# Kernel optimization log

Hardware: AMD Instinct MI355X
Metric: run time of the kernel (lower is better)

The kernel has to match this reference:

```python
import jax, jax.numpy as jnp
import numpy as np

B, T, D_MODEL, D_HIDDEN, MAX_SEQLEN = 4, 2048, 1024, 256, 2048


def setup_inputs() -> dict:
    key = jax.random.key(0)
    ks = jax.random.split(key, 8)
    s_in = 1.0 / np.sqrt(D_MODEL)
    s_out = 1.0 / np.sqrt(D_HIDDEN)
    # xavier_uniform bound for W_bias (fan_in = fan_out = MAX_SEQLEN)
    xb = np.sqrt(6.0 / (MAX_SEQLEN + MAX_SEQLEN))
    return {
        "q": jax.random.normal(ks[0], (B, T, D_MODEL), jnp.float32),
        "k": jax.random.normal(ks[1], (B, T, D_MODEL), jnp.float32),
        "v": jax.random.normal(ks[2], (B, T, D_MODEL), jnp.float32),
        "Wq": jax.random.normal(ks[3], (D_MODEL, D_HIDDEN), jnp.float32) * s_in,
        "Wk": jax.random.normal(ks[4], (D_MODEL, D_HIDDEN), jnp.float32) * s_in,
        "Wv": jax.random.normal(ks[5], (D_MODEL, D_HIDDEN), jnp.float32) * s_in,
        "Wo": jax.random.normal(ks[6], (D_HIDDEN, D_MODEL), jnp.float32) * s_out,
        "W_bias": jax.random.uniform(ks[7], (MAX_SEQLEN, MAX_SEQLEN), jnp.float32, -xb, xb),
    }


def reference(q, k, v, Wq, Wk, Wv, Wo, W_bias):
    Ti, Tj = q.shape[1], k.shape[1]
    Q = q @ Wq                      # [B,Ti,dh]
    K = k @ Wk                      # [B,Tj,dh]
    V = v @ Wv                      # [B,Tj,dh]
    pos_bias = W_bias[:Ti, :Tj][None]               # [1,Ti,Tj]
    # NOTE: source subtracts max over dim 0 (batch). For pos_bias that dim is 1,
    # so exp_pos_bias == exp(0) == ones -- reproduced faithfully here.
    max_key = jnp.max(K, axis=0, keepdims=True)      # [1,Tj,dh]
    max_pos_bias = jnp.max(pos_bias, axis=0, keepdims=True)
    exp_key = jnp.exp(K - max_key)                   # [B,Tj,dh]
    exp_pos_bias = jnp.exp(pos_bias - max_pos_bias)  # [1,Ti,Tj]
    num = jnp.einsum('ij,bjd->bid', exp_pos_bias[0], exp_key * V)  # [B,Ti,dh]
    den = jnp.einsum('ij,bjd->bid', exp_pos_bias[0], exp_key)      # [B,Ti,dh]
    Yt = jax.nn.sigmoid(Q) * num / den
    return Yt @ Wo                  # [B,Ti,d_model]
```

## Files before the change

kernel.cpp:

```cpp
#include <hip/hip_runtime.h>
#include <hip/hip_bf16.h>
#include <math.h>

#define B_   4
#define T_   2048
#define DM   1024
#define DH   256
#define M_   (B_*T_)

typedef __bf16 bf16;
typedef __attribute__((ext_vector_type(8))) __bf16 bf16x8;
typedef __attribute__((ext_vector_type(4))) float  f32x4;

__device__ inline float sigmoidf_(float x) { return 1.0f / (1.0f + __expf(-x)); }

__device__ inline int swz8(int r, int c) { return (((c >> 3) ^ (r & 7)) << 3); }

__global__ void transpose_cvt_all(const float* __restrict__ Wq, const float* __restrict__ Wk,
                                  const float* __restrict__ Wv, const float* __restrict__ Wo,
                                  bf16* __restrict__ Wq_t, bf16* __restrict__ Wk_t,
                                  bf16* __restrict__ Wv_t, bf16* __restrict__ Wo_t)
{
    const int bid = blockIdx.x;
    __shared__ float tile[32][33];
    const int w = bid >> 8, t = bid & 255;
    const float* in; bf16* out; int R, C, sh;
    if      (w == 0) { in = Wq; out = Wq_t; R = DM; C = DH; sh = 3; }
    else if (w == 1) { in = Wk; out = Wk_t; R = DM; C = DH; sh = 3; }
    else if (w == 2) { in = Wv; out = Wv_t; R = DM; C = DH; sh = 3; }
    else             { in = Wo; out = Wo_t; R = DH; C = DM; sh = 5; }
    const int r0 = (t >> sh) * 32, c0 = (t & ((1 << sh) - 1)) * 32;
    const int tx = threadIdx.x & 31, ty = threadIdx.x >> 5;
    #pragma unroll
    for (int i = ty; i < 32; i += 8)
        tile[i][tx] = in[(long)(r0 + i) * C + c0 + tx];
    __syncthreads();
    #pragma unroll
    for (int i = ty; i < 32; i += 8)
        out[(long)(c0 + i) * R + r0 + tx] = (bf16)tile[tx][i];
}

#define GEMM_PHASE(APTR, WT, ACC) {                                           \
    const float* aBase = &(APTR)[arowg * DM + ac8];                           \
    const bf16*  bBase = &(WT)[(long)(n0 + br) * DM + bc16];                  \
    f32x4 pa0[2], pa1[2]; bf16x8 pb0[2], pb1[2];                              \
    _Pragma("unroll")                                                         \
    for (int p = 0; p < 2; ++p) {                                             \
        const float* ap = aBase + p * 64;                                     \
        pa0[p] = *(const f32x4*)ap; pa1[p] = *(const f32x4*)(ap + 4);         \
        const bf16* bp = bBase + p * 64;                                      \
        pb0[p] = *(const bf16x8*)bp; pb1[p] = *(const bf16x8*)(bp + 8);       \
    }                                                                         \
    {   bf16x8 o;                                                             \
        _Pragma("unroll")                                                     \
        for (int e = 0; e < 4; ++e) { o[e] = (bf16)pa0[0][e]; o[4+e] = (bf16)pa1[0][e]; } \
        *(bf16x8*)&As[0][ar][swz8(ar, ac8)]      = o;                         \
        *(bf16x8*)&Bs[0][br][swz8(br, bc16)]     = pb0[0];                    \
        *(bf16x8*)&Bs[0][br][swz8(br, bc16 + 8)] = pb1[0];                    \
    }                                                                         \
    __syncthreads();                                                          \
    _Pragma("unroll")                                                         \
    for (int s = 0; s < 16; ++s) {                                            \
        const int cs = s & 1, ns = cs ^ 1;                                    \
        if (s + 2 < 16) {                                                     \
            const float* ap = aBase + (s + 2) * 64;                           \
            pa0[cs] = *(const f32x4*)ap; pa1[cs] = *(const f32x4*)(ap + 4);   \
            const bf16* bp = bBase + (s + 2) * 64;                            \
            pb0[cs] = *(const bf16x8*)bp; pb1[cs] = *(const bf16x8*)(bp + 8); \
        }                                                                     \
        if (s + 1 < 16) {                                                     \
            bf16x8 o;                                                         \
            _Pragma("unroll")                                                 \
            for (int e = 0; e < 4; ++e) { o[e] = (bf16)pa0[ns][e]; o[4+e] = (bf16)pa1[ns][e]; } \
            *(bf16x8*)&As[ns][ar][swz8(ar, ac8)]      = o;                    \
            *(bf16x8*)&Bs[ns][br][swz8(br, bc16)]     = pb0[ns];              \
            *(bf16x8*)&Bs[ns][br][swz8(br, bc16 + 8)] = pb1[ns];              \
        }                                                                     \
        _Pragma("unroll")                                                     \
        for (int kk = 0; kk < 64; kk += 32) {                                 \
            const int ra = wr * 32 + l16, rb = wc * 32 + l16;                 \
            bf16x8 a0 = *(const bf16x8*)&As[cs][ra     ][swz8(ra,      kk + q4 * 8)]; \
            bf16x8 a1 = *(const bf16x8*)&As[cs][ra + 16][swz8(ra + 16, kk + q4 * 8)]; \
            bf16x8 b0 = *(const bf16x8*)&Bs[cs][rb     ][swz8(rb,      kk + q4 * 8)]; \
            bf16x8 b1 = *(const bf16x8*)&Bs[cs][rb + 16][swz8(rb + 16, kk + q4 * 8)]; \
            ACC[0][0] = __builtin_amdgcn_mfma_f32_16x16x32_bf16(a0, b0, ACC[0][0], 0, 0, 0); \
            ACC[0][1] = __builtin_amdgcn_mfma_f32_16x16x32_bf16(a0, b1, ACC[0][1], 0, 0, 0); \
            ACC[1][0] = __builtin_amdgcn_mfma_f32_16x16x32_bf16(a1, b0, ACC[1][0], 0, 0, 0); \
            ACC[1][1] = __builtin_amdgcn_mfma_f32_16x16x32_bf16(a1, b1, ACC[1][1], 0, 0, 0); \
        }                                                                     \
        __syncthreads();                                                      \
    } }

__global__ __launch_bounds__(512, 6)
void proj_fused(const float* __restrict__ qin, const float* __restrict__ kin,
                const float* __restrict__ vin,
                const bf16* __restrict__ Wq_t, const bf16* __restrict__ Wk_t,
                const bf16* __restrict__ Wv_t,
                bf16* __restrict__ Yb, float* __restrict__ part_num,
                float* __restrict__ part_den)
{
    __shared__ __align__(16) char smem[49152];
    auto As = reinterpret_cast<bf16 (*)[64][64]>(smem);
    auto Bs = reinterpret_cast<bf16 (*)[128][64]>(smem + 16384);

    const int z   = blockIdx.z;
    const int bid = blockIdx.x;
    const int tile = (bid & 7) * 32 + (bid >> 3);
    const int n0 = (tile & 1) * 128;

    const int tid = threadIdx.x, lane = tid & 63, wave = tid >> 6;
    const int wr = wave >> 2, wc = wave & 3;
    const int q4 = lane >> 4, l16 = lane & 15;
    const int ar = tid >> 3, ac8 = (tid & 7) * 8;
    const int br = tid >> 2, bc16 = (tid & 3) * 16;

    const int m0 = (tile >> 1) * 64;
    const int jt = tile >> 1;
    const long arowg = (z == 0) ? (long)(m0 + ar)
                                : (long)(ar >> 4) * T_ + jt * 16 + (ar & 15);

    f32x4 accA[2][2] = {};
    f32x4 accV[2][2] = {};

    if (z == 0) {
        GEMM_PHASE(qin, Wq_t, accA)
        #pragma unroll
        for (int i = 0; i < 2; ++i)
            #pragma unroll
            for (int j = 0; j < 2; ++j)
                #pragma unroll
                for (int r = 0; r < 4; ++r) {
                    int gm = m0 + wr * 32 + i * 16 + q4 * 4 + r;
                    int gn = n0 + wc * 32 + j * 16 + l16;
                    Yb[(long)gm * DH + gn] = (bf16)sigmoidf_(accA[i][j][r]);
                }
    } else {
        GEMM_PHASE(kin, Wk_t, accA)
        GEMM_PHASE(vin, Wv_t, accV)
        auto KL = reinterpret_cast<bf16 (*)[128]>(smem);
        auto VL = reinterpret_cast<bf16 (*)[128]>(smem + 16384);
        float* red_n = (float*)(smem + 32768);
        float* red_d = (float*)(smem + 40960);
        #pragma unroll
        for (int i = 0; i < 2; ++i)
            #pragma unroll
            for (int j = 0; j < 2; ++j)
                #pragma unroll
                for (int r = 0; r < 4; ++r) {
                    const int row = wr * 32 + i * 16 + q4 * 4 + r;
                    const int col = wc * 32 + j * 16 + l16;
                    KL[row][col] = (bf16)accA[i][j][r];
                    VL[row][col] = (bf16)accV[i][j][r];
                }
        __syncthreads();
        const int d = tid & 127, grp = tid >> 7;
        float sn0 = 0.f, sn1 = 0.f, sn2 = 0.f, sn3 = 0.f;
        float sd0 = 0.f, sd1 = 0.f, sd2 = 0.f, sd3 = 0.f;
        #pragma unroll
        for (int jj4 = 0; jj4 < 4; ++jj4) {
            const int jjj = grp * 4 + jj4;
            float k0 = (float)KL[jjj][d],      k1 = (float)KL[16 + jjj][d];
            float k2 = (float)KL[32 + jjj][d], k3 = (float)KL[48 + jjj][d];
            float mx = fmaxf(fmaxf(k0, k1), fmaxf(k2, k3));
            float e0 = __expf(k0 - mx), e1 = __expf(k1 - mx);
            float e2 = __expf(k2 - mx), e3 = __expf(k3 - mx);
            sn0 += e0 * (float)VL[jjj][d];      sd0 += e0;
            sn1 += e1 * (float)VL[16 + jjj][d]; sd1 += e1;
            sn2 += e2 * (float)VL[32 + jjj][d]; sd2 += e2;
            sn3 += e3 * (float)VL[48 + jjj][d]; sd3 += e3;
        }
        red_n[(grp * 4 + 0) * 128 + d] = sn0; red_d[(grp * 4 + 0) * 128 + d] = sd0;
        red_n[(grp * 4 + 1) * 128 + d] = sn1; red_d[(grp * 4 + 1) * 128 + d] = sd1;
        red_n[(grp * 4 + 2) * 128 + d] = sn2; red_d[(grp * 4 + 2) * 128 + d] = sd2;
        red_n[(grp * 4 + 3) * 128 + d] = sn3; red_d[(grp * 4 + 3) * 128 + d] = sd3;
        __syncthreads();
        {
            const int b = tid >> 7, dd = tid & 127;
            float num = red_n[(b) * 128 + dd]      + red_n[(4 + b) * 128 + dd]
                      + red_n[(8 + b) * 128 + dd]  + red_n[(12 + b) * 128 + dd];
            float den = red_d[(b) * 128 + dd]      + red_d[(4 + b) * 128 + dd]
                      + red_d[(8 + b) * 128 + dd]  + red_d[(12 + b) * 128 + dd];
            const int idx = ((jt * 4 + b) << 8) + n0 + dd;
            part_num[idx] = num;
            part_den[idx] = den;
        }
    }
}

__global__ void merge_kv(const float* __restrict__ pn, const float* __restrict__ pd,
                         float* __restrict__ rv)
{
    const int t = blockIdx.x * 256 + threadIdx.x;
    const int b = t >> 8, d = t & 255;
    float num = 0.f, den = 0.f;
    for (int jt = 0; jt < 128; ++jt) {
        num += pn[((jt * 4 + b) << 8) + d];
        den += pd[((jt * 4 + b) << 8) + d];
    }
    rv[t] = num / den;
}

__global__ __launch_bounds__(512, 6)
void gemm_out(const bf16* __restrict__ Yb, const bf16* __restrict__ Wo_t,
              const float* __restrict__ rv, float* __restrict__ out)
{
    __shared__ __align__(16) bf16 As[2][64][64];
    __shared__ __align__(16) bf16 Bs[2][128][64];
    __shared__ float rv_s[DH];

    const int bid  = blockIdx.x;
    const int tile = (bid & 7) * 128 + (bid >> 3);
    const int m0 = (tile >> 3) * 64;
    const int n0 = (tile & 7) * 128;
    const int b  = m0 >> 11;

    const int tid = threadIdx.x, lane = tid & 63, wave = tid >> 6;
    const int wr = wave >> 2, wc = wave & 3;
    const int q4 = lane >> 4, l16 = lane & 15;

    if (tid < DH) rv_s[tid] = rv[b * DH + tid];

    f32x4 acc[2][2] = {};
    const int ar = tid >> 3, ac8 = (tid & 7) * 8;
    const int br = tid >> 2, bc16 = (tid & 3) * 16;

    const bf16* aBase = &Yb[(long)(m0 + ar) * DH + ac8];
    const bf16* bBase = &Wo_t[(long)(n0 + br) * DH + bc16];

    bf16x8 pq[2], pb0[2], pb1[2];
    #pragma unroll
    for (int p = 0; p < 2; ++p) {
        pq[p]  = *(const bf16x8*)(aBase + p * 64);
        const bf16* wp = bBase + p * 64;
        pb0[p] = *(const bf16x8*)wp; pb1[p] = *(const bf16x8*)(wp + 8);
    }
    __syncthreads();
    {
        bf16x8 o;
        #pragma unroll
        for (int e = 0; e < 8; ++e)
            o[e] = (bf16)((float)pq[0][e] * rv_s[ac8 + e]);
        *(bf16x8*)&As[0][ar][swz8(ar, ac8)]      = o;
        *(bf16x8*)&Bs[0][br][swz8(br, bc16)]     = pb0[0];
        *(bf16x8*)&Bs[0][br][swz8(br, bc16 + 8)] = pb1[0];
    }
    __syncthreads();

    #pragma unroll
    for (int s = 0; s < 4; ++s) {
        const int cs = s & 1, ns = cs ^ 1;
        if (s + 2 < 4) {
            pq[cs]  = *(const bf16x8*)(aBase + (s + 2) * 64);
            const bf16* wp = bBase + (s + 2) * 64;
            pb0[cs] = *(const bf16x8*)wp; pb1[cs] = *(const bf16x8*)(wp + 8);
        }
        if (s + 1 < 4) {
            bf16x8 o;
            #pragma unroll
            for (int e = 0; e < 8; ++e)
                o[e] = (bf16)((float)pq[ns][e] * rv_s[(s + 1) * 64 + ac8 + e]);
            *(bf16x8*)&As[ns][ar][swz8(ar, ac8)]      = o;
            *(bf16x8*)&Bs[ns][br][swz8(br, bc16)]     = pb0[ns];
            *(bf16x8*)&Bs[ns][br][swz8(br, bc16 + 8)] = pb1[ns];
        }
        #pragma unroll
        for (int kk = 0; kk < 64; kk += 32) {
            const int ra = wr * 32 + l16, rb = wc * 32 + l16;
            bf16x8 a0 = *(const bf16x8*)&As[cs][ra     ][swz8(ra,      kk + q4 * 8)];
            bf16x8 a1 = *(const bf16x8*)&As[cs][ra + 16][swz8(ra + 16, kk + q4 * 8)];
            bf16x8 b0 = *(const bf16x8*)&Bs[cs][rb     ][swz8(rb,      kk + q4 * 8)];
            bf16x8 b1 = *(const bf16x8*)&Bs[cs][rb + 16][swz8(rb + 16, kk + q4 * 8)];
            acc[0][0] = __builtin_amdgcn_mfma_f32_16x16x32_bf16(a0, b0, acc[0][0], 0, 0, 0);
            acc[0][1] = __builtin_amdgcn_mfma_f32_16x16x32_bf16(a0, b1, acc[0][1], 0, 0, 0);
            acc[1][0] = __builtin_amdgcn_mfma_f32_16x16x32_bf16(a1, b0, acc[1][0], 0, 0, 0);
            acc[1][1] = __builtin_amdgcn_mfma_f32_16x16x32_bf16(a1, b1, acc[1][1], 0, 0, 0);
        }
        __syncthreads();
    }
    #pragma unroll
    for (int i = 0; i < 2; ++i)
        #pragma unroll
        for (int j = 0; j < 2; ++j)
            #pragma unroll
            for (int r = 0; r < 4; ++r) {
                int gm = m0 + wr * 32 + i * 16 + q4 * 4 + r;
                int gn = n0 + wc * 32 + j * 16 + l16;
                out[(long)gm * DM + gn] = acc[i][j][r];
            }
}

extern "C" void kernel_launch(void* const* d_in, const int* in_sizes, int n_in,
                              void* d_out, int out_size, void* d_ws, size_t ws_size,
                              hipStream_t stream)
{
    const float* q  = (const float*)d_in[0];
    const float* k  = (const float*)d_in[1];
    const float* v  = (const float*)d_in[2];
    const float* Wq = (const float*)d_in[3];
    const float* Wk = (const float*)d_in[4];
    const float* Wv = (const float*)d_in[5];
    const float* Wo = (const float*)d_in[6];
    float* out = (float*)d_out;

    char* ws = (char*)d_ws;
    bf16* Yb       = (bf16*)ws;  ws += (size_t)M_ * DH * sizeof(bf16);
    bf16* Wq_t     = (bf16*)ws;  ws += (size_t)DM * DH * sizeof(bf16);
    bf16* Wk_t     = (bf16*)ws;  ws += (size_t)DM * DH * sizeof(bf16);
    bf16* Wv_t     = (bf16*)ws;  ws += (size_t)DM * DH * sizeof(bf16);
    bf16* Wo_t     = (bf16*)ws;  ws += (size_t)DM * DH * sizeof(bf16);
    float* rv      = (float*)ws; ws += (size_t)B_ * DH * sizeof(float);
    float* part_n  = (float*)ws; ws += (size_t)128 * 4 * 256 * sizeof(float);
    float* part_d  = (float*)ws; ws += (size_t)128 * 4 * 256 * sizeof(float);

    transpose_cvt_all<<<1024, 256, 0, stream>>>(Wq, Wk, Wv, Wo,
                                                Wq_t, Wk_t, Wv_t, Wo_t);

    proj_fused<<<dim3(256, 1, 2), 512, 0, stream>>>(q, k, v, Wq_t, Wk_t, Wv_t,
                                                    Yb, part_n, part_d);
    merge_kv<<<4, 256, 0, stream>>>(part_n, part_d, rv);
    gemm_out<<<1024, 512, 0, stream>>>(Yb, Wo_t, rv, out);
}
```

Measured before the change: 195.9 us.

## Shrink GEMM N-tile to 64 to double block count and occupancy

Both the projection kernel and the output GEMM move from 64x128 tiles to 64x64 tiles, so the grids double (512x2 and 2048 blocks) and each wave issues 2 MFMAs per k-step instead of 4. Shared memory per block falls to 32KB and launch bounds rise to 8 blocks per CU, aiming for more parallelism and latency hiding on a chip with many CUs. The K/V reduction epilogue is reworked for the 64-column tile, and the z index that selects the Q path versus the K/V path is swapped. The cost is that the fp32 A-operand inputs (q, k, v) are reloaded and re-converted twice as often, and arithmetic intensity per block is lower.

```diff
diff --git a/kernel.cpp b/kernel.cpp
--- a/kernel.cpp
+++ b/kernel.cpp
@@ -40,23 +40,21 @@
         out[(long)(c0 + i) * R + r0 + tx] = (bf16)tile[tx][i];
 }
 
-#define GEMM_PHASE(APTR, WT, ACC) {                                           \
+#define GEMM_PHASE64(APTR, WT, ACC) {                                         \
     const float* aBase = &(APTR)[arowg * DM + ac8];                           \
-    const bf16*  bBase = &(WT)[(long)(n0 + br) * DM + bc16];                  \
-    f32x4 pa0[2], pa1[2]; bf16x8 pb0[2], pb1[2];                              \
+    const bf16*  bBase = &(WT)[(long)(n0 + ar) * DM + ac8];                   \
+    f32x4 pa0[2], pa1[2]; bf16x8 pb[2];                                       \
     _Pragma("unroll")                                                         \
     for (int p = 0; p < 2; ++p) {                                             \
         const float* ap = aBase + p * 64;                                     \
         pa0[p] = *(const f32x4*)ap; pa1[p] = *(const f32x4*)(ap + 4);         \
-        const bf16* bp = bBase + p * 64;                                      \
-        pb0[p] = *(const bf16x8*)bp; pb1[p] = *(const bf16x8*)(bp + 8);       \
+        pb[p]  = *(const bf16x8*)(bBase + p * 64);                            \
     }                                                                         \
     {   bf16x8 o;                                                             \
         _Pragma("unroll")                                                     \
         for (int e = 0; e < 4; ++e) { o[e] = (bf16)pa0[0][e]; o[4+e] = (bf16)pa1[0][e]; } \
-        *(bf16x8*)&As[0][ar][swz8(ar, ac8)]      = o;                         \
-        *(bf16x8*)&Bs[0][br][swz8(br, bc16)]     = pb0[0];                    \
-        *(bf16x8*)&Bs[0][br][swz8(br, bc16 + 8)] = pb1[0];                    \
+        *(bf16x8*)&As[0][ar][swz8(ar, ac8)] = o;                              \
+        *(bf16x8*)&Bs[0][ar][swz8(ar, ac8)] = pb[0];                          \
     }                                                                         \
     __syncthreads();                                                          \
     _Pragma("unroll")                                                         \
@@ -65,33 +63,28 @@
         if (s + 2 < 16) {                                                     \
             const float* ap = aBase + (s + 2) * 64;                           \
             pa0[cs] = *(const f32x4*)ap; pa1[cs] = *(const f32x4*)(ap + 4);   \
-            const bf16* bp = bBase + (s + 2) * 64;                            \
-            pb0[cs] = *(const bf16x8*)bp; pb1[cs] = *(const bf16x8*)(bp + 8); \
+            pb[cs]  = *(const bf16x8*)(bBase + (s + 2) * 64);                 \
         }                                                                     \
         if (s + 1 < 16) {                                                     \
             bf16x8 o;                                                         \
             _Pragma("unroll")                                                 \
             for (int e = 0; e < 4; ++e) { o[e] = (bf16)pa0[ns][e]; o[4+e] = (bf16)pa1[ns][e]; } \
-            *(bf16x8*)&As[ns][ar][swz8(ar, ac8)]      = o;                    \
-            *(bf16x8*)&Bs[ns][br][swz8(br, bc16)]     = pb0[ns];              \
-            *(bf16x8*)&Bs[ns][br][swz8(br, bc16 + 8)] = pb1[ns];              \
+            *(bf16x8*)&As[ns][ar][swz8(ar, ac8)] = o;                         \
+            *(bf16x8*)&Bs[ns][ar][swz8(ar, ac8)] = pb[ns];                    \
         }                                                                     \
         _Pragma("unroll")                                                     \
         for (int kk = 0; kk < 64; kk += 32) {                                 \
-            const int ra = wr * 32 + l16, rb = wc * 32 + l16;                 \
+            const int ra = wr * 32 + l16, rb = wc * 16 + l16;                 \
             bf16x8 a0 = *(const bf16x8*)&As[cs][ra     ][swz8(ra,      kk + q4 * 8)]; \
             bf16x8 a1 = *(const bf16x8*)&As[cs][ra + 16][swz8(ra + 16, kk + q4 * 8)]; \
             bf16x8 b0 = *(const bf16x8*)&Bs[cs][rb     ][swz8(rb,      kk + q4 * 8)]; \
-            bf16x8 b1 = *(const bf16x8*)&Bs[cs][rb + 16][swz8(rb + 16, kk + q4 * 8)]; \
-            ACC[0][0] = __builtin_amdgcn_mfma_f32_16x16x32_bf16(a0, b0, ACC[0][0], 0, 0, 0); \
-            ACC[0][1] = __builtin_amdgcn_mfma_f32_16x16x32_bf16(a0, b1, ACC[0][1], 0, 0, 0); \
-            ACC[1][0] = __builtin_amdgcn_mfma_f32_16x16x32_bf16(a1, b0, ACC[1][0], 0, 0, 0); \
-            ACC[1][1] = __builtin_amdgcn_mfma_f32_16x16x32_bf16(a1, b1, ACC[1][1], 0, 0, 0); \
+            ACC[0] = __builtin_amdgcn_mfma_f32_16x16x32_bf16(a0, b0, ACC[0], 0, 0, 0); \
+            ACC[1] = __builtin_amdgcn_mfma_f32_16x16x32_bf16(a1, b0, ACC[1], 0, 0, 0); \
         }                                                                     \
         __syncthreads();                                                      \
     } }
 
-__global__ __launch_bounds__(512, 6)
+__global__ __launch_bounds__(512, 8)
 void proj_fused(const float* __restrict__ qin, const float* __restrict__ kin,
                 const float* __restrict__ vin,
                 const bf16* __restrict__ Wq_t, const bf16* __restrict__ Wk_t,
@@ -99,87 +92,84 @@
                 bf16* __restrict__ Yb, float* __restrict__ part_num,
                 float* __restrict__ part_den)
 {
-    __shared__ __align__(16) char smem[49152];
+    __shared__ __align__(16) char smem[32768];
     auto As = reinterpret_cast<bf16 (*)[64][64]>(smem);
-    auto Bs = reinterpret_cast<bf16 (*)[128][64]>(smem + 16384);
+    auto Bs = reinterpret_cast<bf16 (*)[64][64]>(smem + 16384);
 
     const int z   = blockIdx.z;
     const int bid = blockIdx.x;
-    const int tile = (bid & 7) * 32 + (bid >> 3);
-    const int n0 = (tile & 1) * 128;
+    const int tile = (bid & 7) * 64 + (bid >> 3);
+    const int n0 = (tile & 3) * 64;
 
     const int tid = threadIdx.x, lane = tid & 63, wave = tid >> 6;
     const int wr = wave >> 2, wc = wave & 3;
     const int q4 = lane >> 4, l16 = lane & 15;
     const int ar = tid >> 3, ac8 = (tid & 7) * 8;
-    const int br = tid >> 2, bc16 = (tid & 3) * 16;
-
-    const int m0 = (tile >> 1) * 64;
-    const int jt = tile >> 1;
-    const long arowg = (z == 0) ? (long)(m0 + ar)
+
+    const int m0 = (tile >> 2) * 64;
+    const int jt = tile >> 2;
+    const long arowg = (z == 1) ? (long)(m0 + ar)
                                 : (long)(ar >> 4) * T_ + jt * 16 + (ar & 15);
 
-    f32x4 accA[2][2] = {};
-    f32x4 accV[2][2] = {};
-
-    if (z == 0) {
-        GEMM_PHASE(qin, Wq_t, accA)
+    f32x4 accA[2] = {};
+    f32x4 accV[2] = {};
+
+    if (z == 1) {
+        GEMM_PHASE64(qin, Wq_t, accA)
         #pragma unroll
         for (int i = 0; i < 2; ++i)
             #pragma unroll
-            for (int j = 0; j < 2; ++j)
-                #pragma unroll
-                for (int r = 0; r < 4; ++r) {
-                    int gm = m0 + wr * 32 + i * 16 + q4 * 4 + r;
-                    int gn = n0 + wc * 32 + j * 16 + l16;
-                    Yb[(long)gm * DH + gn] = (bf16)sigmoidf_(accA[i][j][r]);
-                }
+            for (int r = 0; r < 4; ++r) {
+                int gm = m0 + wr * 32 + i * 16 + q4 * 4 + r;
+                int gn = n0 + wc * 16 + l16;
+                Yb[(long)gm * DH + gn] = (bf16)sigmoidf_(accA[i][r]);
+            }
     } else {
-        GEMM_PHASE(kin, Wk_t, accA)
-        GEMM_PHASE(vin, Wv_t, accV)
-        auto KL = reinterpret_cast<bf16 (*)[128]>(smem);
-        auto VL = reinterpret_cast<bf16 (*)[128]>(smem + 16384);
-        float* red_n = (float*)(smem + 32768);
-        float* red_d = (float*)(smem + 40960);
+        GEMM_PHASE64(kin, Wk_t, accA)
+        GEMM_PHASE64(vin, Wv_t, accV)
+        auto KL = reinterpret_cast<bf16 (*)[64]>(smem);
+        auto VL = reinterpret_cast<bf16 (*)[64]>(smem + 8192);
+        float* red_n = (float*)(smem + 16384);
+        float* red_d = (float*)(smem + 24576);
         #pragma unroll
         for (int i = 0; i < 2; ++i)
             #pragma unroll
-            for (int j = 0; j < 2; ++j)
-                #pragma unroll
-                for (int r = 0; r < 4; ++r) {
-                    const int row = wr * 32 + i * 16 + q4 * 4 + r;
-                    const int col = wc * 32 + j * 16 + l16;
-                    KL[row][col] = (bf16)accA[i][j][r];
-                    VL[row][col] = (bf16)accV[i][j][r];
-                }
+            for (int r = 0; r < 4; ++r) {
+                const int row = wr * 32 + i * 16 + q4 * 4 + r;
+                const int col = wc * 16 + l16;
+                KL[row][col] = (bf16)accA[i][r];
+                VL[row][col] = (bf16)accV[i][r];
+            }
         __syncthreads();
-        const int d = tid & 127, grp = tid >> 7;
-        float sn0 = 0.f, sn1 = 0.f, sn2 = 0.f, sn3 = 0.f;
-        float sd0 = 0.f, sd1 = 0.f, sd2 = 0.f, sd3 = 0.f;
-        #pragma unroll
-        for (int jj4 = 0; jj4 < 4; ++jj4) {
-            const int jjj = grp * 4 + jj4;
-            float k0 = (float)KL[jjj][d],      k1 = (float)KL[16 + jjj][d];
-            float k2 = (float)KL[32 + jjj][d], k3 = (float)KL[48 + jjj][d];
+        const int d = tid & 63, grp = tid >> 6;
+        float sn[B_] = {}, sd[B_] = {};
+        #pragma unroll
+        for (int jj2 = 0; jj2 < 2; ++jj2) {
+            const int jj = grp * 2 + jj2;
+            float k0 = (float)KL[jj][d],      k1 = (float)KL[16 + jj][d];
+            float k2 = (float)KL[32 + jj][d], k3 = (float)KL[48 + jj][d];
             float mx = fmaxf(fmaxf(k0, k1), fmaxf(k2, k3));
             float e0 = __expf(k0 - mx), e1 = __expf(k1 - mx);
             float e2 = __expf(k2 - mx), e3 = __expf(k3 - mx);
-            sn0 += e0 * (float)VL[jjj][d];      sd0 += e0;
-            sn1 += e1 * (float)VL[16 + jjj][d]; sd1 += e1;
-            sn2 += e2 * (float)VL[32 + jjj][d]; sd2 += e2;
-            sn3 += e3 * (float)VL[48 + jjj][d]; sd3 += e3;
-        }
-        red_n[(grp * 4 + 0) * 128 + d] = sn0; red_d[(grp * 4 + 0) * 128 + d] = sd0;
-        red_n[(grp * 4 + 1) * 128 + d] = sn1; red_d[(grp * 4 + 1) * 128 + d] = sd1;
-        red_n[(grp * 4 + 2) * 128 + d] = sn2; red_d[(grp * 4 + 2) * 128 + d] = sd2;
-        red_n[(grp * 4 + 3) * 128 + d] = sn3; red_d[(grp * 4 + 3) * 128 + d] = sd3;
+            sn[0] += e0 * (float)VL[jj][d];      sd[0] += e0;
+            sn[1] += e1 * (float)VL[16 + jj][d]; sd[1] += e1;
+            sn[2] += e2 * (float)VL[32 + jj][d]; sd[2] += e2;
+            sn[3] += e3 * (float)VL[48 + jj][d]; sd[3] += e3;
+        }
+        #pragma unroll
+        for (int b = 0; b < B_; ++b) {
+            red_n[(b * 8 + grp) * 64 + d] = sn[b];
+            red_d[(b * 8 + grp) * 64 + d] = sd[b];
+        }
         __syncthreads();
-        {
-            const int b = tid >> 7, dd = tid & 127;
-            float num = red_n[(b) * 128 + dd]      + red_n[(4 + b) * 128 + dd]
-                      + red_n[(8 + b) * 128 + dd]  + red_n[(12 + b) * 128 + dd];
-            float den = red_d[(b) * 128 + dd]      + red_d[(4 + b) * 128 + dd]
-                      + red_d[(8 + b) * 128 + dd]  + red_d[(12 + b) * 128 + dd];
+        if (tid < 256) {
+            const int b = tid >> 6, dd = tid & 63;
+            float num = 0.f, den = 0.f;
+            #pragma unroll
+            for (int g = 0; g < 8; ++g) {
+                num += red_n[(b * 8 + g) * 64 + dd];
+                den += red_d[(b * 8 + g) * 64 + dd];
+            }
             const int idx = ((jt * 4 + b) << 8) + n0 + dd;
             part_num[idx] = num;
             part_den[idx] = den;
@@ -200,39 +190,38 @@
     rv[t] = num / den;
 }
 
-__global__ __launch_bounds__(512, 6)
+__global__ __launch_bounds__(512, 8)
 void gemm_out(const bf16* __restrict__ Yb, const bf16* __restrict__ Wo_t,
               const float* __restrict__ rv, float* __restrict__ out)
 {
-    __shared__ __align__(16) bf16 As[2][64][64];
-    __shared__ __align__(16) bf16 Bs[2][128][64];
+    __shared__ __align__(16) char smem[32768];
+    auto As = reinterpret_cast<bf16 (*)[64][64]>(smem);
+    auto Bs = reinterpret_cast<bf16 (*)[64][64]>(smem + 16384);
     __shared__ float rv_s[DH];
 
     const int bid  = blockIdx.x;
-    const int tile = (bid & 7) * 128 + (bid >> 3);
-    const int m0 = (tile >> 3) * 64;
-    const int n0 = (tile & 7) * 128;
+    const int tile = (bid & 7) * 256 + (bid >> 3);
+    const int m0 = (tile >> 4) * 64;
+    const int n0 = (tile & 15) * 64;
     const int b  = m0 >> 11;
 
     const int tid = threadIdx.x, lane = tid & 63, wave = tid >> 6;
     const int wr = wave >> 2, wc = wave & 3;
     const int q4 = lane >> 4, l16 = lane & 15;
+    const int ar = tid >> 3, ac8 = (tid & 7) * 8;
 
     if (tid < DH) rv_s[tid] = rv[b * DH + tid];
 
-    f32x4 acc[2][2] = {};
-    const int ar = tid >> 3, ac8 = (tid & 7) * 8;
-    const int br = tid >> 2, bc16 = (tid & 3) * 16;
+    f32x4 acc[2] = {};
 
     const bf16* aBase = &Yb[(long)(m0 + ar) * DH + ac8];
-    const bf16* bBase = &Wo_t[(long)(n0 + br) * DH + bc16];
-
-    bf16x8 pq[2], pb0[2], pb1[2];
+    const bf16* bBase = &Wo_t[(long)(n0 + ar) * DH + ac8];
+
+    bf16x8 pq[2], pb[2];
     #pragma unroll
     for (int p = 0; p < 2; ++p) {
-        pq[p]  = *(const bf16x8*)(aBase + p * 64);
-        const bf16* wp = bBase + p * 64;
-        pb0[p] = *(const bf16x8*)wp; pb1[p] = *(const bf16x8*)(wp + 8);
+        pq[p] = *(const bf16x8*)(aBase + p * 64);
+        pb[p] = *(const bf16x8*)(bBase + p * 64);
     }
     __syncthreads();
     {
@@ -240,9 +229,8 @@
         #pragma unroll
         for (int e = 0; e < 8; ++e)
             o[e] = (bf16)((float)pq[0][e] * rv_s[ac8 + e]);
-        *(bf16x8*)&As[0][ar][swz8(ar, ac8)]      = o;
-        *(bf16x8*)&Bs[0][br][swz8(br, bc16)]     = pb0[0];
-        *(bf16x8*)&Bs[0][br][swz8(br, bc16 + 8)] = pb1[0];
+        *(bf16x8*)&As[0][ar][swz8(ar, ac8)] = o;
+        *(bf16x8*)&Bs[0][ar][swz8(ar, ac8)] = pb[0];
     }
     __syncthreads();
 
@@ -250,43 +238,36 @@
     for (int s = 0; s < 4; ++s) {
         const int cs = s & 1, ns = cs ^ 1;
         if (s + 2 < 4) {
-            pq[cs]  = *(const bf16x8*)(aBase + (s + 2) * 64);
-            const bf16* wp = bBase + (s + 2) * 64;
-            pb0[cs] = *(const bf16x8*)wp; pb1[cs] = *(const bf16x8*)(wp + 8);
+            pq[cs] = *(const bf16x8*)(aBase + (s + 2) * 64);
+            pb[cs] = *(const bf16x8*)(bBase + (s + 2) * 64);
         }
         if (s + 1 < 4) {
             bf16x8 o;
             #pragma unroll
             for (int e = 0; e < 8; ++e)
                 o[e] = (bf16)((float)pq[ns][e] * rv_s[(s + 1) * 64 + ac8 + e]);
-            *(bf16x8*)&As[ns][ar][swz8(ar, ac8)]      = o;
-            *(bf16x8*)&Bs[ns][br][swz8(br, bc16)]     = pb0[ns];
-            *(bf16x8*)&Bs[ns][br][swz8(br, bc16 + 8)] = pb1[ns];
+            *(bf16x8*)&As[ns][ar][swz8(ar, ac8)] = o;
+            *(bf16x8*)&Bs[ns][ar][swz8(ar, ac8)] = pb[ns];
         }
         #pragma unroll
         for (int kk = 0; kk < 64; kk += 32) {
-            const int ra = wr * 32 + l16, rb = wc * 32 + l16;
+            const int ra = wr * 32 + l16, rb = wc * 16 + l16;
             bf16x8 a0 = *(const bf16x8*)&As[cs][ra     ][swz8(ra,      kk + q4 * 8)];
             bf16x8 a1 = *(const bf16x8*)&As[cs][ra + 16][swz8(ra + 16, kk + q4 * 8)];
             bf16x8 b0 = *(const bf16x8*)&Bs[cs][rb     ][swz8(rb,      kk + q4 * 8)];
-            bf16x8 b1 = *(const bf16x8*)&Bs[cs][rb + 16][swz8(rb + 16, kk + q4 * 8)];
-            acc[0][0] = __builtin_amdgcn_mfma_f32_16x16x32_bf16(a0, b0, acc[0][0], 0, 0, 0);
-            acc[0][1] = __builtin_amdgcn_mfma_f32_16x16x32_bf16(a0, b1, acc[0][1], 0, 0, 0);
-            acc[1][0] = __builtin_amdgcn_mfma_f32_16x16x32_bf16(a1, b0, acc[1][0], 0, 0, 0);
-            acc[1][1] = __builtin_amdgcn_mfma_f32_16x16x32_bf16(a1, b1, acc[1][1], 0, 0, 0);
+            acc[0] = __builtin_amdgcn_mfma_f32_16x16x32_bf16(a0, b0, acc[0], 0, 0, 0);
+            acc[1] = __builtin_amdgcn_mfma_f32_16x16x32_bf16(a1, b0, acc[1], 0, 0, 0);
         }
         __syncthreads();
     }
     #pragma unroll
     for (int i = 0; i < 2; ++i)
         #pragma unroll
-        for (int j = 0; j < 2; ++j)
-            #pragma unroll
-            for (int r = 0; r < 4; ++r) {
-                int gm = m0 + wr * 32 + i * 16 + q4 * 4 + r;
-                int gn = n0 + wc * 32 + j * 16 + l16;
-                out[(long)gm * DM + gn] = acc[i][j][r];
-            }
+        for (int r = 0; r < 4; ++r) {
+            int gm = m0 + wr * 32 + i * 16 + q4 * 4 + r;
+            int gn = n0 + wc * 16 + l16;
+            out[(long)gm * DM + gn] = acc[i][r];
+        }
 }
 
 extern "C" void kernel_launch(void* const* d_in, const int* in_sizes, int n_in,
@@ -315,8 +296,8 @@
     transpose_cvt_all<<<1024, 256, 0, stream>>>(Wq, Wk, Wv, Wo,
                                                 Wq_t, Wk_t, Wv_t, Wo_t);
 
-    proj_fused<<<dim3(256, 1, 2), 512, 0, stream>>>(q, k, v, Wq_t, Wk_t, Wv_t,
+    proj_fused<<<dim3(512, 1, 2), 512, 0, stream>>>(q, k, v, Wq_t, Wk_t, Wv_t,
                                                     Yb, part_n, part_d);
     merge_kv<<<4, 256, 0, stream>>>(part_n, part_d, rv);
-    gemm_out<<<1024, 512, 0, stream>>>(Yb, Wo_t, rv, out);
-}
+    gemm_out<<<2048, 512, 0, stream>>>(Yb, Wo_t, rv, out);
+}
```

Measured after the change: 211.2 us. 1.08x slower.
